# Kernel optimization log

Hardware: AMD Instinct MI355X
Metric: run time of the kernel (lower is better)

## Reference

```python
import jax, jax.numpy as jnp
import numpy as np

NUM_HEADS = 10
DICT = 20  # attention_dictionary_size
BATCH = 262144


def setup_inputs() -> dict:
    key = jax.random.key(0)
    ks = jax.random.split(key, 6)
    x = jax.random.normal(ks[0], (BATCH, DICT), dtype=jnp.float32)
    # torch nn.Linear(20, 200, bias=False) weights: shape [out, in] = [200, 20]
    W1 = jax.random.normal(ks[1], (NUM_HEADS * DICT, DICT), dtype=jnp.float32) * 0.1
    W2 = jax.random.normal(ks[2], (NUM_HEADS * DICT, DICT), dtype=jnp.float32) * 0.1
    W3 = jax.random.normal(ks[3], (NUM_HEADS * DICT, DICT), dtype=jnp.float32) * 0.1
    W4 = jax.random.normal(ks[4], (NUM_HEADS * DICT, DICT), dtype=jnp.float32) * 0.1
    gamma = jax.random.normal(ks[5], (1,), dtype=jnp.float32)
    return {"x": x, "W1": W1, "W2": W2, "W3": W3, "W4": W4, "gamma": gamma}


def reference(x, W1, W2, W3, W4, gamma):
    B = x.shape[0]
    m = 1
    inp = x[:, None, :]                                   # [B, 1, 20]
    # Four bias-free projections: y = x @ W.T -> [B, 1, 200]
    q = (inp @ W1.T).reshape(NUM_HEADS, B, m, DICT)       # faithful .view (mixes batch/head)
    k = (inp @ W2.T).reshape(NUM_HEADS, B, DICT, m)
    v = (inp @ W3.T).reshape(NUM_HEADS, B, m, DICT)
    inner = q @ k                                         # [10, B, 1, 1]
    att = jax.nn.softmax(inner, axis=-1)                  # length-1 softmax -> ones (faithful)
    res = jnp.swapaxes(att, -1, -2) @ v                   # [10, B, 1, 20]
    res = res.reshape(B, m, NUM_HEADS * DICT)             # [B, 1, 200]
    out = jax.nn.relu(gamma * res + inp @ W4.T)           # [B, 1, 200]
    return out
```

## Files before the change

kernel.cpp:

```cpp
#include <hip/hip_runtime.h>


#define BATCH          262144
#define DICT           20
#define COLS           200
#define NTHREADS       256
#define ROWS_PER_BLOCK 128
#define ROWS_PER_WAVE  32
#define NBLOCKS        (BATCH / ROWS_PER_BLOCK)

typedef float f32x4 __attribute__((ext_vector_type(4)));

__global__ __launch_bounds__(NTHREADS, 3)
void attn_v6_kernel(const float* __restrict__ x,
                    const float* __restrict__ W3,
                    const float* __restrict__ W4,
                    const float* __restrict__ gamma,
                    float* __restrict__ out)
{
    __shared__ f32x4 ldsX[ROWS_PER_BLOCK * 5];

    const int t = threadIdx.x;

    const f32x4* xg = (const f32x4*)(x + (size_t)blockIdx.x * ROWS_PER_BLOCK * DICT);
    for (int i = t; i < ROWS_PER_BLOCK * 5; i += NTHREADS)
        ldsX[i] = __builtin_nontemporal_load(&xg[i]);
    __syncthreads();

    const int lane = t & 63;
    const int wv   = t >> 6;
    if (lane >= 50) return;

    const float g   = gamma[0];
    const int   cf4 = lane;

    f32x4 m[4][5];
#pragma unroll
    for (int c = 0; c < 4; ++c) {
        const f32x4* a = (const f32x4*)(W3 + (4 * cf4 + c) * DICT);
        const f32x4* b = (const f32x4*)(W4 + (4 * cf4 + c) * DICT);
#pragma unroll
        for (int k = 0; k < 5; ++k) {
            f32x4 p = a[k], q = b[k], r;
            r.x = fmaf(g, p.x, q.x); r.y = fmaf(g, p.y, q.y);
            r.z = fmaf(g, p.z, q.z); r.w = fmaf(g, p.w, q.w);
            m[c][k] = r;
        }
    }

    const int row0 = blockIdx.x * ROWS_PER_BLOCK + wv * ROWS_PER_WAVE;
    const f32x4* xl = &ldsX[wv * ROWS_PER_WAVE * 5];
    f32x4* op = (f32x4*)(out + (size_t)row0 * COLS) + cf4;

#define DOT4(ACC, XV)                                          \
    {                                                          \
        float* ap_ = (float*)&(ACC);                           \
        _Pragma("unroll")                                      \
        for (int c = 0; c < 4; ++c) {                          \
            float p0 = 0.f, p1 = 0.f;                          \
            _Pragma("unroll")                                  \
            for (int k = 0; k < 5; ++k) {                      \
                p0 = fmaf(m[c][k].x, (XV)[k].x, p0);           \
                p1 = fmaf(m[c][k].y, (XV)[k].y, p1);           \
                p0 = fmaf(m[c][k].z, (XV)[k].z, p0);           \
                p1 = fmaf(m[c][k].w, (XV)[k].w, p1);           \
            }                                                  \
            ap_[c] = fmaxf(p0 + p1, 0.f);                      \
        }                                                      \
    }

    f32x4 xv[5], xn[5];
#pragma unroll
    for (int k = 0; k < 5; ++k) xv[k] = xl[k];

    for (int r = 0; r < ROWS_PER_WAVE; r += 2) {
#pragma unroll
        for (int k = 0; k < 5; ++k) xn[k] = xl[(r + 1) * 5 + k];

        f32x4 acc0;
        DOT4(acc0, xv)
        __builtin_nontemporal_store(acc0, &op[(size_t)r * 50]);

        if (r + 2 < ROWS_PER_WAVE) {
#pragma unroll
            for (int k = 0; k < 5; ++k) xv[k] = xl[(r + 2) * 5 + k];
        }

        f32x4 acc1;
        DOT4(acc1, xn)
        __builtin_nontemporal_store(acc1, &op[(size_t)(r + 1) * 50]);
    }
#undef DOT4
}

extern "C" void kernel_launch(void* const* d_in, const int* in_sizes, int n_in,
                              void* d_out, int out_size, void* d_ws, size_t ws_size,
                              hipStream_t stream) {
    const float* x     = (const float*)d_in[0];
    const float* W3    = (const float*)d_in[3];
    const float* W4    = (const float*)d_in[4];
    const float* gamma = (const float*)d_in[5];
    float* out = (float*)d_out;

    attn_v6_kernel<<<NBLOCKS, NTHREADS, 0, stream>>>(x, W3, W4, gamma, out);
}
```

Before: 248.3 us.

## Read x rows via scalar constant-address loads instead of LDS staging

Removes the shared-memory staging of x and the block-wide barrier. Each wave instead reads its rows through an address_space(4) pointer with a wave-uniform base, so the compiler can emit scalar (SMEM) loads that are broadcast to all lanes. The occupancy hint in launch_bounds is raised from 3 to 4. The cost is a dependence on the scalar data cache and on scalar load latency, with no explicit prefetch of the next row pair.

```diff
diff --git a/kernel.cpp b/kernel.cpp
--- a/kernel.cpp
+++ b/kernel.cpp
@@ -10,25 +10,36 @@
 #define NBLOCKS        (BATCH / ROWS_PER_BLOCK)
 
 typedef float f32x4 __attribute__((ext_vector_type(4)));
+typedef const float __attribute__((address_space(4))) kfloat;
 
-__global__ __launch_bounds__(NTHREADS, 3)
-void attn_v6_kernel(const float* __restrict__ x,
+#define DOT_S(ACC, XS)                                        \
+    {                                                         \
+        float* ap_ = (float*)&(ACC);                          \
+        _Pragma("unroll")                                     \
+        for (int c = 0; c < 4; ++c) {                         \
+            float p0 = 0.f, p1 = 0.f;                         \
+            _Pragma("unroll")                                 \
+            for (int k = 0; k < 5; ++k) {                     \
+                p0 = fmaf(m[c][k].x, (XS)[4 * k + 0], p0);    \
+                p1 = fmaf(m[c][k].y, (XS)[4 * k + 1], p1);    \
+                p0 = fmaf(m[c][k].z, (XS)[4 * k + 2], p0);    \
+                p1 = fmaf(m[c][k].w, (XS)[4 * k + 3], p1);    \
+            }                                                 \
+            ap_[c] = fmaxf(p0 + p1, 0.f);                     \
+        }                                                     \
+    }
+
+__global__ __launch_bounds__(NTHREADS, 4)
+void attn_v8_kernel(const float* __restrict__ x,
                     const float* __restrict__ W3,
                     const float* __restrict__ W4,
                     const float* __restrict__ gamma,
                     float* __restrict__ out)
 {
-    __shared__ f32x4 ldsX[ROWS_PER_BLOCK * 5];
+    const int t    = threadIdx.x;
+    const int lane = t & 63;
+    const int wvu  = __builtin_amdgcn_readfirstlane(t >> 6);
 
-    const int t = threadIdx.x;
-
-    const f32x4* xg = (const f32x4*)(x + (size_t)blockIdx.x * ROWS_PER_BLOCK * DICT);
-    for (int i = t; i < ROWS_PER_BLOCK * 5; i += NTHREADS)
-        ldsX[i] = __builtin_nontemporal_load(&xg[i]);
-    __syncthreads();
-
-    const int lane = t & 63;
-    const int wv   = t >> 6;
     if (lane >= 50) return;
 
     const float g   = gamma[0];
@@ -48,49 +59,25 @@
         }
     }
 
-    const int row0 = blockIdx.x * ROWS_PER_BLOCK + wv * ROWS_PER_WAVE;
-    const f32x4* xl = &ldsX[wv * ROWS_PER_WAVE * 5];
-    f32x4* op = (f32x4*)(out + (size_t)row0 * COLS) + cf4;
-
-#define DOT4(ACC, XV)                                          \
-    {                                                          \
-        float* ap_ = (float*)&(ACC);                           \
-        _Pragma("unroll")                                      \
-        for (int c = 0; c < 4; ++c) {                          \
-            float p0 = 0.f, p1 = 0.f;                          \
-            _Pragma("unroll")                                  \
-            for (int k = 0; k < 5; ++k) {                      \
-                p0 = fmaf(m[c][k].x, (XV)[k].x, p0);           \
-                p1 = fmaf(m[c][k].y, (XV)[k].y, p1);           \
-                p0 = fmaf(m[c][k].z, (XV)[k].z, p0);           \
-                p1 = fmaf(m[c][k].w, (XV)[k].w, p1);           \
-            }                                                  \
-            ap_[c] = fmaxf(p0 + p1, 0.f);                      \
-        }                                                      \
-    }
-
-    f32x4 xv[5], xn[5];
-#pragma unroll
-    for (int k = 0; k < 5; ++k) xv[k] = xl[k];
+    const int row_base = blockIdx.x * ROWS_PER_BLOCK + wvu * ROWS_PER_WAVE;
+    kfloat* xc = (kfloat*)(size_t)(x + (size_t)row_base * DICT);
+    f32x4*  op = (f32x4*)(out + (size_t)row_base * COLS) + cf4;
 
     for (int r = 0; r < ROWS_PER_WAVE; r += 2) {
+        float xs0[DICT], xs1[DICT];
 #pragma unroll
-        for (int k = 0; k < 5; ++k) xn[k] = xl[(r + 1) * 5 + k];
+        for (int k = 0; k < DICT; ++k) xs0[k] = xc[r * DICT + k];
+#pragma unroll
+        for (int k = 0; k < DICT; ++k) xs1[k] = xc[(r + 1) * DICT + k];
 
         f32x4 acc0;
-        DOT4(acc0, xv)
+        DOT_S(acc0, xs0)
         __builtin_nontemporal_store(acc0, &op[(size_t)r * 50]);
 
-        if (r + 2 < ROWS_PER_WAVE) {
-#pragma unroll
-            for (int k = 0; k < 5; ++k) xv[k] = xl[(r + 2) * 5 + k];
-        }
-
         f32x4 acc1;
-        DOT4(acc1, xn)
+        DOT_S(acc1, xs1)
         __builtin_nontemporal_store(acc1, &op[(size_t)(r + 1) * 50]);
     }
-#undef DOT4
 }
 
 extern "C" void kernel_launch(void* const* d_in, const int* in_sizes, int n_in,
@@ -102,5 +89,5 @@
     const float* gamma = (const float*)d_in[5];
     float* out = (float*)d_out;
 
-    attn_v6_kernel<<<NBLOCKS, NTHREADS, 0, stream>>>(x, W3, W4, gamma, out);
+    attn_v8_kernel<<<NBLOCKS, NTHREADS, 0, stream>>>(x, W3, W4, gamma, out);
 }
```

Result: slower. 259.3 us (+4.4%).
